# Kernel optimization log

Hardware: AMD Instinct MI355X
Metric: run time of the kernel (lower is better)

The kernel has to match this reference:

```python
import jax, jax.numpy as jnp
import numpy as np

NUM_CLASSES = 80
STRIDE = 8
IMG_SIZE = 640
BOX_W, OBJ_W, CLS_W = 7.5, 1.0, 0.5
ANCHORS = jnp.array([[10.0, 13.0], [16.0, 30.0], [33.0, 23.0]], dtype=jnp.float32)
EPS_IOU = 1e-9
EPS_CIOU = 1e-7


def setup_inputs() -> dict:
    key = jax.random.key(0)
    k1, k2, k3 = jax.random.split(key, 3)
    B, na, H, W, D = 16, 3, 80, 80, 5 + NUM_CLASSES
    N = 48  # objects per image
    p_raw = jax.random.normal(k1, (B, na, H, W, D), dtype=jnp.float32)
    labels_xywh = jax.random.uniform(k2, (B, N, 4), dtype=jnp.float32)  # normalized (xc,yc,w,h)
    labels_cls = jax.random.randint(k3, (B, N), 0, NUM_CLASSES, dtype=jnp.int32)
    return {"p_raw": p_raw, "labels_xywh": labels_xywh, "labels_cls": labels_cls}


def _assign_targets(labels_cls, labels_xywh, B, na, H, W):
    lab = labels_xywh * IMG_SIZE  # [B,N,4] in pixels
    gx, gy, gw, gh = lab[..., 0], lab[..., 1], lab[..., 2], lab[..., 3]
    gi_idx = jnp.clip(gx / STRIDE, 0, W - 0.001).astype(jnp.int32)  # [B,N]
    gj_idx = jnp.clip(gy / STRIDE, 0, H - 0.001).astype(jnp.int32)
    a_wh = ANCHORS / STRIDE  # [na,2] anchors in grid units
    gtw, gth = gw / STRIDE, gh / STRIDE
    inter = jnp.minimum(gtw[..., None], a_wh[:, 0]) * jnp.minimum(gth[..., None], a_wh[:, 1])
    union = gtw[..., None] * gth[..., None] + a_wh[:, 0] * a_wh[:, 1] - inter + EPS_IOU
    best_a = jnp.argmax(inter / union, axis=-1).astype(jnp.int32)  # [B,N]

    # 3x3 neighborhood offsets (di over x, dj over y), matching torch loop order
    offs = jnp.array([(di, dj) for di in (-1, 0, 1) for dj in (-1, 0, 1)], dtype=jnp.int32)  # [9,2]
    bidx = jnp.arange(B, dtype=jnp.int32)

    tobj = jnp.zeros((B, na, H, W), dtype=jnp.float32)
    tcls = jnp.zeros((B, na, H, W, NUM_CLASSES), dtype=jnp.float32)
    tbox = jnp.zeros((B, na, H, W, 4), dtype=jnp.float32)

    def step(carry, x):
        tobj, tcls, tbox = carry
        a, gi, gj, c, box = x  # a,gi,gj,c: [B]; box: [B,4]
        ii = jnp.clip(gi[:, None] + offs[None, :, 0], 0, W - 1)  # [B,9]
        jj = jnp.clip(gj[:, None] + offs[None, :, 1], 0, H - 1)  # [B,9]
        b9 = jnp.broadcast_to(bidx[:, None], (B, 9))
        a9 = jnp.broadcast_to(a[:, None], (B, 9))
        c9 = jnp.broadcast_to(c[:, None], (B, 9))
        tobj = tobj.at[b9, a9, jj, ii].set(1.0)
        tcls = tcls.at[b9, a9, jj, ii, c9].set(1.0)
        tbox = tbox.at[b9, a9, jj, ii].set(jnp.broadcast_to(box[:, None, :], (B, 9, 4)))
        return (tobj, tcls, tbox), None

    xs = (best_a.T, gi_idx.T, gj_idx.T, labels_cls.T, jnp.swapaxes(lab, 0, 1))
    (tobj, tcls, tbox), _ = jax.lax.scan(step, (tobj, tcls, tbox), xs)
    return tobj, tcls, tbox


def _ciou(pred, tgt):
    # pred, tgt: [..., 4] (xc, yc, w, h) in pixels
    px, py, pw, ph = pred[..., 0], pred[..., 1], pred[..., 2], pred[..., 3]
    gx, gy, gw, gh = tgt[..., 0], tgt[..., 1], tgt[..., 2], tgt[..., 3]
    px1, py1, px2, py2 = px - pw / 2, py - ph / 2, px + pw / 2, py + ph / 2
    gx1, gy1, gx2, gy2 = gx - gw / 2, gy - gh / 2, gx + gw / 2, gy + gh / 2
    iw = jnp.clip(jnp.minimum(px2, gx2) - jnp.maximum(px1, gx1), 0)
    ih = jnp.clip(jnp.minimum(py2, gy2) - jnp.maximum(py1, gy1), 0)
    inter = iw * ih
    area_p = jnp.clip(px2 - px1, 0) * jnp.clip(py2 - py1, 0)
    area_g = jnp.clip(gx2 - gx1, 0) * jnp.clip(gy2 - gy1, 0)
    union = area_p + area_g - inter + EPS_CIOU
    iou = inter / union
    cw = jnp.clip(jnp.maximum(px2, gx2) - jnp.minimum(px1, gx1), 0)
    ch = jnp.clip(jnp.maximum(py2, gy2) - jnp.minimum(py1, gy1), 0)
    c2 = cw * cw + ch * ch + EPS_CIOU
    rho2 = (px - gx) ** 2 + (py - gy) ** 2
    v = (4.0 / (np.pi ** 2)) * (jnp.arctan(gw / (gh + EPS_CIOU)) - jnp.arctan(pw / (ph + EPS_CIOU))) ** 2
    alpha = jax.lax.stop_gradient(v / (1 - iou + v + EPS_CIOU))
    return 1 - (iou - rho2 / c2 - alpha * v)


def _bce_logits(x, t):
    # stable binary cross-entropy with logits: softplus(x) - t*x
    return jax.nn.softplus(x) - t * x


def reference(p_raw, labels_xywh, labels_cls):
    B, na, H, W, D = p_raw.shape
    ag = ANCHORS / STRIDE  # anchors in grid units
    px = jax.nn.sigmoid(p_raw[..., 0])
    py = jax.nn.sigmoid(p_raw[..., 1])
    pw = jnp.exp(p_raw[..., 2]) * ag[:, 0][None, :, None, None]
    ph = jnp.exp(p_raw[..., 3]) * ag[:, 1][None, :, None, None]
    logits_obj = p_raw[..., 4]
    logits_cls = p_raw[..., 5:]

    gyv, gxv = jnp.meshgrid(jnp.arange(H, dtype=jnp.float32), jnp.arange(W, dtype=jnp.float32), indexing='ij')
    gx = (gxv[None, None] + px) * STRIDE
    gy = (gyv[None, None] + py) * STRIDE
    pxywh = jnp.stack([gx, gy, pw * STRIDE, ph * STRIDE], -1)  # [B,na,H,W,4]

    tobj, tcls, tbox = _assign_targets(labels_cls, labels_xywh, B, na, H, W)
    pos = tobj > 0.5
    n_pos = jnp.maximum(jnp.sum(pos), 1).astype(jnp.float32)

    ciou = _ciou(pxywh, tbox)  # [B,na,H,W]
    l_box = jnp.sum(jnp.where(pos, ciou, 0.0)) / n_pos
    l_obj = jnp.mean(_bce_logits(logits_obj, tobj))
    bce_cls = _bce_logits(logits_cls, tcls)  # [B,na,H,W,nc]
    l_cls = jnp.sum(jnp.where(pos[..., None], bce_cls, 0.0)) / (n_pos * NUM_CLASSES)

    total = BOX_W * l_box + OBJ_W * l_obj + CLS_W * l_cls
    return total
```

## Files before the change

kernel.cpp:

```cpp
#include <hip/hip_runtime.h>

#define NC    80
#define B_    16
#define NA    3
#define HW    80
#define D_    85
#define NLAB  48
#define NCELL  (B_*NA*HW*HW)
#define OBJBLK (NCELL/256)
#define POSBLK (B_*108)

__device__ __forceinline__ float softplusf(float x) {
    return fmaxf(x, 0.f) + log1pf(expf(-fabsf(x)));
}
__device__ __forceinline__ int clampi(int v, int lo, int hi) {
    return min(max(v, lo), hi);
}

__global__ __launch_bounds__(256) void k_obj(const float* __restrict__ p,
                                             float* __restrict__ opart) {
    int t = threadIdx.x;
    int idx = blockIdx.x * 256 + t;
    float s = softplusf(p[(size_t)idx * D_ + 4]);
    #pragma unroll
    for (int o = 32; o; o >>= 1) s += __shfl_xor(s, o);
    __shared__ float ws[4];
    if ((t & 63) == 0) ws[t >> 6] = s;
    __syncthreads();
    if (t == 0) opart[blockIdx.x] = ws[0] + ws[1] + ws[2] + ws[3];
}

__global__ __launch_bounds__(256) void k_pos(const float* __restrict__ p,
                                             const float* __restrict__ lx,
                                             const int*   __restrict__ lc,
                                             float* __restrict__ ppart) {
    int t = threadIdx.x, lane = t & 63, wid = t >> 6;
    int pb = blockIdx.x;
    int b  = pb / 108;

    __shared__ float Lgx[NLAB], Lgy[NLAB], Lgw[NLAB], Lgh[NLAB];
    __shared__ int   Lgi[NLAB], Lgj[NLAB], La[NLAB], Lc[NLAB];

    if (t < NLAB) {
        float4 L = ((const float4*)lx)[b * NLAB + t];
        float gx = L.x * 640.f, gy = L.y * 640.f;
        float gw = L.z * 640.f, gh = L.w * 640.f;
        Lgx[t] = gx; Lgy[t] = gy; Lgw[t] = gw; Lgh[t] = gh;
        Lgi[t] = (int)fminf(fmaxf(gx * 0.125f, 0.f), 79.999f);
        Lgj[t] = (int)fminf(fmaxf(gy * 0.125f, 0.f), 79.999f);
        float gtw = gw * 0.125f, gth = gh * 0.125f;
        const float aw[3] = {1.25f, 2.0f, 4.125f};
        const float ah[3] = {1.625f, 3.75f, 2.875f};
        int a = 0; float best = -1.f;
        #pragma unroll
        for (int k = 0; k < 3; k++) {
            float inter = fminf(gtw, aw[k]) * fminf(gth, ah[k]);
            float uni   = gtw * gth + aw[k] * ah[k] - inter + 1e-9f;
            float r = inter / uni;
            if (r > best) { best = r; a = k; }
        }
        La[t] = a;
        Lc[t] = lc[b * NLAB + t];
    }
    __syncthreads();

    int cand = (pb % 108) * 4 + wid;
    int n = cand / 9, off = cand % 9;
    int gi = Lgi[n], gj = Lgj[n], a = La[n];
    int ii = clampi(gi + off / 3 - 1, 0, 79);
    int jj = clampi(gj + off % 3 - 1, 0, 79);

    bool viol = false;
    if (lane < 9) {
        if (lane < off) {
            int i2 = clampi(gi + lane / 3 - 1, 0, 79);
            int j2 = clampi(gj + lane % 3 - 1, 0, 79);
            viol = (i2 == ii) && (j2 == jj);
        }
    } else {
        int n2 = n + 1 + (lane - 9);
        if (n2 < NLAB && La[n2] == a) {
            int g2 = Lgi[n2], h2 = Lgj[n2];
            viol = ii >= max(g2 - 1, 0) && ii <= min(g2 + 1, 79) &&
                   jj >= max(h2 - 1, 0) && jj <= min(h2 + 1, 79);
        }
    }
    bool own = (__ballot(viol) == 0ull);

    float box = 0.f, cls = 0.f, xc = 0.f, npf = 0.f;
    if (own) {
        int cell = ((b * NA + a) * HW + jj) * HW + ii;
        const float* pc = p + (size_t)cell * D_;
        int c = Lc[n];

        float x = pc[5 + lane];
        float cs = softplusf(x) - ((lane == c) ? x : 0.f);
        if (lane < 16) {
            float x2 = pc[69 + lane];
            cs += softplusf(x2) - ((lane + 64 == c) ? x2 : 0.f);
        }
        #pragma unroll
        for (int o = 32; o; o >>= 1) cs += __shfl_xor(cs, o);

        if (lane == 0) {
            npf = 1.f;
            cls = cs;
            xc  = pc[4];

            float awv = (a == 0) ? 10.f : ((a == 1) ? 16.f : 33.f);
            float ahv = (a == 0) ? 13.f : ((a == 1) ? 30.f : 23.f);
            float p0 = pc[0], p1 = pc[1], p2 = pc[2], p3 = pc[3];
            float sx = 1.f / (1.f + expf(-p0));
            float sy = 1.f / (1.f + expf(-p1));
            float px = ((float)ii + sx) * 8.f;
            float py = ((float)jj + sy) * 8.f;
            float pw = expf(p2) * awv;
            float ph = expf(p3) * ahv;

            float gx = Lgx[n], gy = Lgy[n], gw = Lgw[n], gh = Lgh[n];

            float px1 = px - pw * 0.5f, px2 = px + pw * 0.5f;
            float py1 = py - ph * 0.5f, py2 = py + ph * 0.5f;
            float gx1 = gx - gw * 0.5f, gx2 = gx + gw * 0.5f;
            float gy1 = gy - gh * 0.5f, gy2 = gy + gh * 0.5f;

            float iw = fmaxf(fminf(px2, gx2) - fmaxf(px1, gx1), 0.f);
            float ih = fmaxf(fminf(py2, gy2) - fmaxf(py1, gy1), 0.f);
            float inter = iw * ih;
            float ap = fmaxf(px2 - px1, 0.f) * fmaxf(py2 - py1, 0.f);
            float ag = fmaxf(gx2 - gx1, 0.f) * fmaxf(gy2 - gy1, 0.f);
            float uni = ap + ag - inter + 1e-7f;
            float iou = inter / uni;

            float cw = fmaxf(fmaxf(px2, gx2) - fminf(px1, gx1), 0.f);
            float ch = fmaxf(fmaxf(py2, gy2) - fminf(py1, gy1), 0.f);
            float c2 = cw * cw + ch * ch + 1e-7f;
            float rho2 = (px - gx) * (px - gx) + (py - gy) * (py - gy);

            float dv = atanf(gw / (gh + 1e-7f)) - atanf(pw / (ph + 1e-7f));
            float v = 0.40528473456935108577f * dv * dv;
            float alpha = v / (1.f - iou + v + 1e-7f);
            box = 1.f - (iou - rho2 / c2 - alpha * v);
        }
    }

    __shared__ float r4[4][4];
    if (lane == 0) { r4[wid][0] = box; r4[wid][1] = cls; r4[wid][2] = xc; r4[wid][3] = npf; }
    __syncthreads();
    if (t == 0) {
        float4 o;
        o.x = r4[0][0] + r4[1][0] + r4[2][0] + r4[3][0];
        o.y = r4[0][1] + r4[1][1] + r4[2][1] + r4[3][1];
        o.z = r4[0][2] + r4[1][2] + r4[2][2] + r4[3][2];
        o.w = r4[0][3] + r4[1][3] + r4[2][3] + r4[3][3];
        ((float4*)ppart)[pb] = o;
    }
}

__global__ __launch_bounds__(256) void k_fin(const float* __restrict__ opart,
                                             const float* __restrict__ ppart,
                                             float* __restrict__ out) {
    int t = threadIdx.x, lane = t & 63, wid = t >> 6;
    float o = 0.f, box = 0.f, cls = 0.f, xc = 0.f, np = 0.f;
    #pragma unroll
    for (int k = 0; k < 5; k++) {
        int i = t + k * 256;
        if (i < OBJBLK) o += opart[i];
    }
    #pragma unroll
    for (int k = 0; k < 7; k++) {
        int i = t + k * 256;
        if (i < POSBLK) {
            float4 v = ((const float4*)ppart)[i];
            box += v.x; cls += v.y; xc += v.z; np += v.w;
        }
    }
    #pragma unroll
    for (int s = 32; s; s >>= 1) {
        o   += __shfl_xor(o,   s);
        box += __shfl_xor(box, s);
        cls += __shfl_xor(cls, s);
        xc  += __shfl_xor(xc,  s);
        np  += __shfl_xor(np,  s);
    }
    __shared__ float r[4][5];
    if (lane == 0) { r[wid][0]=o; r[wid][1]=box; r[wid][2]=cls; r[wid][3]=xc; r[wid][4]=np; }
    __syncthreads();
    if (t == 0) {
        float O  = r[0][0] + r[1][0] + r[2][0] + r[3][0];
        float Bx = r[0][1] + r[1][1] + r[2][1] + r[3][1];
        float Cl = r[0][2] + r[1][2] + r[2][2] + r[3][2];
        float Xc = r[0][3] + r[1][3] + r[2][3] + r[3][3];
        float Np = r[0][4] + r[1][4] + r[2][4] + r[3][4];
        float npos = fmaxf(Np, 1.f);
        out[0] = 7.5f * Bx / npos
               + (O - Xc) / (float)NCELL
               + 0.5f * Cl / (npos * (float)NC);
    }
}

extern "C" void kernel_launch(void* const* d_in, const int* in_sizes, int n_in,
                              void* d_out, int out_size, void* d_ws, size_t ws_size,
                              hipStream_t stream) {
    const float* p  = (const float*)d_in[0];
    const float* lx = (const float*)d_in[1];
    const int*   lc = (const int*)d_in[2];
    float*       out = (float*)d_out;

    float* opart = (float*)d_ws;
    float* ppart = (float*)((char*)d_ws + 8192);

    k_obj<<<OBJBLK, 256, 0, stream>>>(p, opart);
    k_pos<<<POSBLK, 256, 0, stream>>>(p, lx, lc, ppart);
    k_fin<<<1, 256, 0, stream>>>(opart, ppart, out);
}
```

Measured before the change: 24.87 us.

## Fuse obj, pos and final reduction into one kernel with last-block atomic

Merges the three kernel launches into a single grid where the low block ids compute the objectness softplus partial sums and the remaining ids compute the positive-cell box and class terms. The block that arrives last, detected with an atomic counter and thread fences, performs the final reduction. The goal is to remove two kernel launch gaps and let the objectness and positive-cell work run concurrently. In exchange it adds a memset launch to reset the counter, plus an atomic and fence in every block.

```diff
diff --git a/kernel.cpp b/kernel.cpp
--- a/kernel.cpp
+++ b/kernel.cpp
@@ -9,6 +9,7 @@
 #define NCELL  (B_*NA*HW*HW)
 #define OBJBLK (NCELL/256)
 #define POSBLK (B_*108)
+#define NBLK_T (OBJBLK+POSBLK)
 
 __device__ __forceinline__ float softplusf(float x) {
     return fmaxf(x, 0.f) + log1pf(expf(-fabsf(x)));
@@ -17,150 +18,157 @@
     return min(max(v, lo), hi);
 }
 
-__global__ __launch_bounds__(256) void k_obj(const float* __restrict__ p,
-                                             float* __restrict__ opart) {
-    int t = threadIdx.x;
-    int idx = blockIdx.x * 256 + t;
-    float s = softplusf(p[(size_t)idx * D_ + 4]);
-    #pragma unroll
-    for (int o = 32; o; o >>= 1) s += __shfl_xor(s, o);
-    __shared__ float ws[4];
-    if ((t & 63) == 0) ws[t >> 6] = s;
-    __syncthreads();
-    if (t == 0) opart[blockIdx.x] = ws[0] + ws[1] + ws[2] + ws[3];
-}
-
-__global__ __launch_bounds__(256) void k_pos(const float* __restrict__ p,
-                                             const float* __restrict__ lx,
-                                             const int*   __restrict__ lc,
-                                             float* __restrict__ ppart) {
-    int t = threadIdx.x, lane = t & 63, wid = t >> 6;
-    int pb = blockIdx.x;
-    int b  = pb / 108;
-
-    __shared__ float Lgx[NLAB], Lgy[NLAB], Lgw[NLAB], Lgh[NLAB];
-    __shared__ int   Lgi[NLAB], Lgj[NLAB], La[NLAB], Lc[NLAB];
-
-    if (t < NLAB) {
-        float4 L = ((const float4*)lx)[b * NLAB + t];
-        float gx = L.x * 640.f, gy = L.y * 640.f;
-        float gw = L.z * 640.f, gh = L.w * 640.f;
-        Lgx[t] = gx; Lgy[t] = gy; Lgw[t] = gw; Lgh[t] = gh;
-        Lgi[t] = (int)fminf(fmaxf(gx * 0.125f, 0.f), 79.999f);
-        Lgj[t] = (int)fminf(fmaxf(gy * 0.125f, 0.f), 79.999f);
-        float gtw = gw * 0.125f, gth = gh * 0.125f;
-        const float aw[3] = {1.25f, 2.0f, 4.125f};
-        const float ah[3] = {1.625f, 3.75f, 2.875f};
-        int a = 0; float best = -1.f;
+__global__ __launch_bounds__(256) void k_main(const float* __restrict__ p,
+                                              const float* __restrict__ lx,
+                                              const int*   __restrict__ lc,
+                                              float* __restrict__ opart,
+                                              float* __restrict__ ppart,
+                                              int*   __restrict__ cnt,
+                                              float* __restrict__ out) {
+    int t = threadIdx.x, bid = blockIdx.x;
+    int lane = t & 63, wid = t >> 6;
+    __shared__ float r4[4][5];
+
+    if (bid < OBJBLK) {
+        int idx = bid * 256 + t;
+        float s = softplusf(p[(size_t)idx * D_ + 4]);
         #pragma unroll
-        for (int k = 0; k < 3; k++) {
-            float inter = fminf(gtw, aw[k]) * fminf(gth, ah[k]);
-            float uni   = gtw * gth + aw[k] * ah[k] - inter + 1e-9f;
-            float r = inter / uni;
-            if (r > best) { best = r; a = k; }
-        }
-        La[t] = a;
-        Lc[t] = lc[b * NLAB + t];
-    }
-    __syncthreads();
-
-    int cand = (pb % 108) * 4 + wid;
-    int n = cand / 9, off = cand % 9;
-    int gi = Lgi[n], gj = Lgj[n], a = La[n];
-    int ii = clampi(gi + off / 3 - 1, 0, 79);
-    int jj = clampi(gj + off % 3 - 1, 0, 79);
-
-    bool viol = false;
-    if (lane < 9) {
-        if (lane < off) {
-            int i2 = clampi(gi + lane / 3 - 1, 0, 79);
-            int j2 = clampi(gj + lane % 3 - 1, 0, 79);
-            viol = (i2 == ii) && (j2 == jj);
-        }
+        for (int o = 32; o; o >>= 1) s += __shfl_xor(s, o);
+        if (lane == 0) r4[wid][0] = s;
+        __syncthreads();
+        if (t == 0) opart[bid] = r4[0][0] + r4[1][0] + r4[2][0] + r4[3][0];
     } else {
-        int n2 = n + 1 + (lane - 9);
-        if (n2 < NLAB && La[n2] == a) {
-            int g2 = Lgi[n2], h2 = Lgj[n2];
-            viol = ii >= max(g2 - 1, 0) && ii <= min(g2 + 1, 79) &&
-                   jj >= max(h2 - 1, 0) && jj <= min(h2 + 1, 79);
-        }
-    }
-    bool own = (__ballot(viol) == 0ull);
-
-    float box = 0.f, cls = 0.f, xc = 0.f, npf = 0.f;
-    if (own) {
-        int cell = ((b * NA + a) * HW + jj) * HW + ii;
-        const float* pc = p + (size_t)cell * D_;
-        int c = Lc[n];
-
-        float x = pc[5 + lane];
-        float cs = softplusf(x) - ((lane == c) ? x : 0.f);
-        if (lane < 16) {
-            float x2 = pc[69 + lane];
-            cs += softplusf(x2) - ((lane + 64 == c) ? x2 : 0.f);
-        }
-        #pragma unroll
-        for (int o = 32; o; o >>= 1) cs += __shfl_xor(cs, o);
-
-        if (lane == 0) {
-            npf = 1.f;
-            cls = cs;
-            xc  = pc[4];
-
-            float awv = (a == 0) ? 10.f : ((a == 1) ? 16.f : 33.f);
-            float ahv = (a == 0) ? 13.f : ((a == 1) ? 30.f : 23.f);
-            float p0 = pc[0], p1 = pc[1], p2 = pc[2], p3 = pc[3];
-            float sx = 1.f / (1.f + expf(-p0));
-            float sy = 1.f / (1.f + expf(-p1));
-            float px = ((float)ii + sx) * 8.f;
-            float py = ((float)jj + sy) * 8.f;
-            float pw = expf(p2) * awv;
-            float ph = expf(p3) * ahv;
-
-            float gx = Lgx[n], gy = Lgy[n], gw = Lgw[n], gh = Lgh[n];
-
-            float px1 = px - pw * 0.5f, px2 = px + pw * 0.5f;
-            float py1 = py - ph * 0.5f, py2 = py + ph * 0.5f;
-            float gx1 = gx - gw * 0.5f, gx2 = gx + gw * 0.5f;
-            float gy1 = gy - gh * 0.5f, gy2 = gy + gh * 0.5f;
-
-            float iw = fmaxf(fminf(px2, gx2) - fmaxf(px1, gx1), 0.f);
-            float ih = fmaxf(fminf(py2, gy2) - fmaxf(py1, gy1), 0.f);
-            float inter = iw * ih;
-            float ap = fmaxf(px2 - px1, 0.f) * fmaxf(py2 - py1, 0.f);
-            float ag = fmaxf(gx2 - gx1, 0.f) * fmaxf(gy2 - gy1, 0.f);
-            float uni = ap + ag - inter + 1e-7f;
-            float iou = inter / uni;
-
-            float cw = fmaxf(fmaxf(px2, gx2) - fminf(px1, gx1), 0.f);
-            float ch = fmaxf(fmaxf(py2, gy2) - fminf(py1, gy1), 0.f);
-            float c2 = cw * cw + ch * ch + 1e-7f;
-            float rho2 = (px - gx) * (px - gx) + (py - gy) * (py - gy);
-
-            float dv = atanf(gw / (gh + 1e-7f)) - atanf(pw / (ph + 1e-7f));
-            float v = 0.40528473456935108577f * dv * dv;
-            float alpha = v / (1.f - iou + v + 1e-7f);
-            box = 1.f - (iou - rho2 / c2 - alpha * v);
-        }
-    }
-
-    __shared__ float r4[4][4];
-    if (lane == 0) { r4[wid][0] = box; r4[wid][1] = cls; r4[wid][2] = xc; r4[wid][3] = npf; }
+        int pb = bid - OBJBLK;
+        int b  = pb / 108;
+
+        __shared__ float Lgx[NLAB], Lgy[NLAB], Lgw[NLAB], Lgh[NLAB];
+        __shared__ int   Lgi[NLAB], Lgj[NLAB], La[NLAB], Lc[NLAB];
+
+        if (t < NLAB) {
+            float4 L = ((const float4*)lx)[b * NLAB + t];
+            float gx = L.x * 640.f, gy = L.y * 640.f;
+            float gw = L.z * 640.f, gh = L.w * 640.f;
+            Lgx[t] = gx; Lgy[t] = gy; Lgw[t] = gw; Lgh[t] = gh;
+            Lgi[t] = (int)fminf(fmaxf(gx * 0.125f, 0.f), 79.999f);
+            Lgj[t] = (int)fminf(fmaxf(gy * 0.125f, 0.f), 79.999f);
+            float gtw = gw * 0.125f, gth = gh * 0.125f;
+            const float aw[3] = {1.25f, 2.0f, 4.125f};
+            const float ah[3] = {1.625f, 3.75f, 2.875f};
+            int a = 0; float best = -1.f;
+            #pragma unroll
+            for (int k = 0; k < 3; k++) {
+                float inter = fminf(gtw, aw[k]) * fminf(gth, ah[k]);
+                float uni   = gtw * gth + aw[k] * ah[k] - inter + 1e-9f;
+                float r = inter / uni;
+                if (r > best) { best = r; a = k; }
+            }
+            La[t] = a;
+            Lc[t] = lc[b * NLAB + t];
+        }
+        __syncthreads();
+
+        int cand = (pb % 108) * 4 + wid;
+        int n = cand / 9, off = cand % 9;
+        int gi = Lgi[n], gj = Lgj[n], a = La[n];
+        int ii = clampi(gi + off / 3 - 1, 0, 79);
+        int jj = clampi(gj + off % 3 - 1, 0, 79);
+
+        bool viol = false;
+        if (lane < 9) {
+            if (lane < off) {
+                int i2 = clampi(gi + lane / 3 - 1, 0, 79);
+                int j2 = clampi(gj + lane % 3 - 1, 0, 79);
+                viol = (i2 == ii) && (j2 == jj);
+            }
+        } else {
+            int n2 = n + 1 + (lane - 9);
+            if (n2 < NLAB && La[n2] == a) {
+                int g2 = Lgi[n2], h2 = Lgj[n2];
+                viol = ii >= max(g2 - 1, 0) && ii <= min(g2 + 1, 79) &&
+                       jj >= max(h2 - 1, 0) && jj <= min(h2 + 1, 79);
+            }
+        }
+        bool own = (__ballot(viol) == 0ull);
+
+        float box = 0.f, cls = 0.f, xc = 0.f, npf = 0.f;
+        if (own) {
+            int cell = ((b * NA + a) * HW + jj) * HW + ii;
+            const float* pc = p + (size_t)cell * D_;
+            int c = Lc[n];
+
+            float x = pc[5 + lane];
+            float cs = softplusf(x) - ((lane == c) ? x : 0.f);
+            if (lane < 16) {
+                float x2 = pc[69 + lane];
+                cs += softplusf(x2) - ((lane + 64 == c) ? x2 : 0.f);
+            }
+            #pragma unroll
+            for (int o = 32; o; o >>= 1) cs += __shfl_xor(cs, o);
+
+            if (lane == 0) {
+                npf = 1.f;
+                cls = cs;
+                xc  = pc[4];
+
+                float awv = (a == 0) ? 10.f : ((a == 1) ? 16.f : 33.f);
+                float ahv = (a == 0) ? 13.f : ((a == 1) ? 30.f : 23.f);
+                float p0 = pc[0], p1 = pc[1], p2 = pc[2], p3 = pc[3];
+                float sx = 1.f / (1.f + expf(-p0));
+                float sy = 1.f / (1.f + expf(-p1));
+                float px = ((float)ii + sx) * 8.f;
+                float py = ((float)jj + sy) * 8.f;
+                float pw = expf(p2) * awv;
+                float ph = expf(p3) * ahv;
+
+                float gx = Lgx[n], gy = Lgy[n], gw = Lgw[n], gh = Lgh[n];
+
+                float px1 = px - pw * 0.5f, px2 = px + pw * 0.5f;
+                float py1 = py - ph * 0.5f, py2 = py + ph * 0.5f;
+                float gx1 = gx - gw * 0.5f, gx2 = gx + gw * 0.5f;
+                float gy1 = gy - gh * 0.5f, gy2 = gy + gh * 0.5f;
+
+                float iw = fmaxf(fminf(px2, gx2) - fmaxf(px1, gx1), 0.f);
+                float ih = fmaxf(fminf(py2, gy2) - fmaxf(py1, gy1), 0.f);
+                float inter = iw * ih;
+                float ap = fmaxf(px2 - px1, 0.f) * fmaxf(py2 - py1, 0.f);
+                float ag = fmaxf(gx2 - gx1, 0.f) * fmaxf(gy2 - gy1, 0.f);
+                float uni = ap + ag - inter + 1e-7f;
+                float iou = inter / uni;
+
+                float cw = fmaxf(fmaxf(px2, gx2) - fminf(px1, gx1), 0.f);
+                float ch = fmaxf(fmaxf(py2, gy2) - fminf(py1, gy1), 0.f);
+                float c2 = cw * cw + ch * ch + 1e-7f;
+                float rho2 = (px - gx) * (px - gx) + (py - gy) * (py - gy);
+
+                float dv = atanf(gw / (gh + 1e-7f)) - atanf(pw / (ph + 1e-7f));
+                float v = 0.40528473456935108577f * dv * dv;
+                float alpha = v / (1.f - iou + v + 1e-7f);
+                box = 1.f - (iou - rho2 / c2 - alpha * v);
+            }
+        }
+
+        if (lane == 0) { r4[wid][0] = box; r4[wid][1] = cls; r4[wid][2] = xc; r4[wid][3] = npf; }
+        __syncthreads();
+        if (t == 0) {
+            float4 o;
+            o.x = r4[0][0] + r4[1][0] + r4[2][0] + r4[3][0];
+            o.y = r4[0][1] + r4[1][1] + r4[2][1] + r4[3][1];
+            o.z = r4[0][2] + r4[1][2] + r4[2][2] + r4[3][2];
+            o.w = r4[0][3] + r4[1][3] + r4[2][3] + r4[3][3];
+            ((float4*)ppart)[pb] = o;
+        }
+    }
+
+    __shared__ bool amLast;
     __syncthreads();
     if (t == 0) {
-        float4 o;
-        o.x = r4[0][0] + r4[1][0] + r4[2][0] + r4[3][0];
-        o.y = r4[0][1] + r4[1][1] + r4[2][1] + r4[3][1];
-        o.z = r4[0][2] + r4[1][2] + r4[2][2] + r4[3][2];
-        o.w = r4[0][3] + r4[1][3] + r4[2][3] + r4[3][3];
-        ((float4*)ppart)[pb] = o;
-    }
-}
-
-__global__ __launch_bounds__(256) void k_fin(const float* __restrict__ opart,
-                                             const float* __restrict__ ppart,
-                                             float* __restrict__ out) {
-    int t = threadIdx.x, lane = t & 63, wid = t >> 6;
+        __threadfence();
+        amLast = (atomicAdd(cnt, 1) == NBLK_T - 1);
+    }
+    __syncthreads();
+    if (!amLast) return;
+    __threadfence();
+
     float o = 0.f, box = 0.f, cls = 0.f, xc = 0.f, np = 0.f;
     #pragma unroll
     for (int k = 0; k < 5; k++) {
@@ -209,8 +217,8 @@
 
     float* opart = (float*)d_ws;
     float* ppart = (float*)((char*)d_ws + 8192);
-
-    k_obj<<<OBJBLK, 256, 0, stream>>>(p, opart);
-    k_pos<<<POSBLK, 256, 0, stream>>>(p, lx, lc, ppart);
-    k_fin<<<1, 256, 0, stream>>>(opart, ppart, out);
-}
+    int*   cnt   = (int*)((char*)d_ws + 8192 + 27648);
+
+    hipMemsetAsync(cnt, 0, 4, stream);
+    k_main<<<NBLK_T, 256, 0, stream>>>(p, lx, lc, opart, ppart, cnt, out);
+}
```

After: 81.06 us. +226.0%, slower.
